# Performance work log

Measured on AMD Instinct MI355X. Metric: run time of the kernel, lower is better.

Reference implementation:

```python
import jax, jax.numpy as jnp
import numpy as np


def setup_inputs() -> dict:
    key = jax.random.key(0)
    ks = jax.random.split(key, 6)
    N, Tx, Ty = 8, 1024, 128
    enc_dim, dec_dim, Ca = 512, 1024, 128
    sc = 0.02
    return {
        "h": jax.random.normal(ks[0], (N, Tx, enc_dim), jnp.float32),
        "s": jax.random.normal(ks[1], (N, Ty, dec_dim), jnp.float32),
        "Wh": jax.random.normal(ks[2], (enc_dim, Ca), jnp.float32) * sc,
        "Ws": jax.random.normal(ks[3], (dec_dim, Ca), jnp.float32) * sc,
        "b": jax.random.normal(ks[4], (Ca,), jnp.float32) * sc,
        "v": jax.random.normal(ks[5], (Ca,), jnp.float32) * sc,
    }


def reference(h, s, Wh, Ws, b, v):
    # W([h;s]) + b == h@Wh + s@Ws + b (split of the concat Linear weight)
    ph = jnp.einsum("nxc,ca->nxa", h, Wh)            # (N, Tx, Ca)
    ps = jnp.einsum("nyd,da->nya", s, Ws) + b        # (N, Ty, Ca)
    # broadcast-add -> tanh -> dot with v : (N, Ty, Tx)
    e = jnp.einsum("nyxa,a->nyx", jnp.tanh(ps[:, :, None, :] + ph[:, None, :, :]), v)
    return jax.nn.softmax(e, axis=-1)                # attention over Tx
```

## Files before the change

kernel.cpp:

```cpp
#include <hip/hip_runtime.h>
#include <stdint.h>


typedef float  f32x4  __attribute__((ext_vector_type(4)));
typedef __bf16 bf16x8 __attribute__((ext_vector_type(8)));

#define LOG2E     1.4426950408889634f
#define TWO_LOG2E 2.8853900817779268f

__global__ void __launch_bounds__(256) transpose_cast(
    const float* __restrict__ Wh, const float* __restrict__ Ws,
    __bf16* __restrict__ WhT, __bf16* __restrict__ WsT)
{
    int bid = blockIdx.x;
    const float* src; __bf16* dst; int K, c0;
    if (bid < 8) { src = Wh; dst = WhT; K = 512;  c0 = bid * 64; }
    else         { src = Ws; dst = WsT; K = 1024; c0 = (bid - 8) * 64; }
    __shared__ float tile[64][129];
    int t = threadIdx.x;
    for (int i = 0; i < 8192; i += 256) {
        int idx = i + t;
        int r = idx >> 7, col = idx & 127;
        tile[r][col] = src[(size_t)(c0 + r) * 128 + col];
    }
    __syncthreads();
    for (int i = 0; i < 8192; i += 256) {
        int idx = i + t;
        int a = idx >> 6, cc = idx & 63;
        dst[(size_t)a * K + c0 + cc] = (__bf16)tile[cc][a];
    }
}

__global__ void __launch_bounds__(256) gemm_fused(
    const __bf16* __restrict__ WhT, const __bf16* __restrict__ WsT,
    const float* __restrict__ h, const float* __restrict__ s,
    float* __restrict__ Eph, float* __restrict__ Eps,
    const float* __restrict__ bias)
{
    int bid = blockIdx.x;
    int tid = threadIdx.x, lane = tid & 63, w = tid >> 6;
    int mbase = (w & 1) * 64;
    const __bf16* A; const float* B; float* Cp; int K; bool isPs;
    int colg;
    if (bid < 256) {
        isPs = false; A = WhT; B = h; K = 512;
        colg = bid * 32 + (w >> 1) * 16;
        int n = colg >> 10, x = colg & 1023;
        Cp = Eph + (size_t)n * 131072 + x;
    } else {
        isPs = true; A = WsT; B = s; K = 1024;
        colg = (bid - 256) * 32 + (w >> 1) * 16;
        Cp = Eps + colg;
    }
    int q = lane >> 4;
    const float*  Bp = B + (size_t)(colg + (lane & 15)) * K + q * 8;
    const __bf16* Ap = A + (size_t)(mbase + (lane & 15)) * K + q * 8;

    f32x4 acc[4] = {};
    float4 b0 = *(const float4*)(Bp);
    float4 b1 = *(const float4*)(Bp + 4);
    bf16x8 a_[4];
    #pragma unroll
    for (int i = 0; i < 4; ++i) a_[i] = *(const bf16x8*)(Ap + (size_t)i * 16 * K);

    for (int k0 = 0; k0 < K; k0 += 32) {
        int kn = k0 + 32; if (kn > K - 32) kn = K - 32;
        float4 nb0 = *(const float4*)(Bp + kn);
        float4 nb1 = *(const float4*)(Bp + kn + 4);
        bf16x8 na[4];
        #pragma unroll
        for (int i = 0; i < 4; ++i)
            na[i] = *(const bf16x8*)(Ap + (size_t)i * 16 * K + kn);
        bf16x8 bf;
        bf[0] = (__bf16)b0.x; bf[1] = (__bf16)b0.y;
        bf[2] = (__bf16)b0.z; bf[3] = (__bf16)b0.w;
        bf[4] = (__bf16)b1.x; bf[5] = (__bf16)b1.y;
        bf[6] = (__bf16)b1.z; bf[7] = (__bf16)b1.w;
        #pragma unroll
        for (int i = 0; i < 4; ++i)
            acc[i] = __builtin_amdgcn_mfma_f32_16x16x32_bf16(a_[i], bf, acc[i], 0, 0, 0);
        b0 = nb0; b1 = nb1;
        #pragma unroll
        for (int i = 0; i < 4; ++i) a_[i] = na[i];
    }

    int col = lane & 15;
    #pragma unroll
    for (int i = 0; i < 4; ++i) {
        #pragma unroll
        for (int r = 0; r < 4; ++r) {
            int m = mbase + i * 16 + q * 4 + r;
            float vv = acc[i][r];
            if (isPs) vv += bias[m];
            Cp[(size_t)m * 1024 + col] =
                __builtin_amdgcn_exp2f(vv * TWO_LOG2E);
        }
    }
}

__global__ void __launch_bounds__(512) attn_softmax(
    const float* __restrict__ Eph, const float* __restrict__ Eps,
    const float* __restrict__ v, float* __restrict__ out)
{
    int bid = blockIdx.x;
    int n = bid >> 6, yg = bid & 63;
    int ny = n * 128 + yg * 2;
    const float2* ph2 = (const float2*)(Eph + (size_t)n * 131072);
    int t = threadIdx.x;

    __shared__ float4 pv_s[128];
    __shared__ float wred[2][8];
    __shared__ float VsumS;

    if (t < 128) {
        float2 p = *(const float2*)(Eps + (size_t)t * 1024 + ny);
        float4 pk; pk.x = p.x; pk.y = p.y; pk.z = v[t]; pk.w = 0.f;
        pv_s[t] = pk;
    }
    if (t >= 448) {
        int l = t - 448;
        float vv = v[l] + v[l + 64];
        for (int m = 32; m; m >>= 1) vv += __shfl_xor(vv, m);
        if (l == 0) VsumS = vv;
    }
    __syncthreads();
    float Vsum = VsumS;

    float acc00 = 0.f, acc01 = 0.f, acc10 = 0.f, acc11 = 0.f;
    #pragma unroll 2
    for (int a = 0; a < 128; a += 4) {
        float4 q0 = pv_s[a + 0], q1 = pv_s[a + 1];
        float4 q2 = pv_s[a + 2], q3 = pv_s[a + 3];
        float2 p0 = ph2[(a + 0) * 512 + t];
        float2 p1 = ph2[(a + 1) * 512 + t];
        float2 p2 = ph2[(a + 2) * 512 + t];
        float2 p3 = ph2[(a + 3) * 512 + t];
        auto comb = [&](float e0, float e1, float e2, float e3,
                        float h0, float h1, float h2, float h3, float& acc) {
            float w0 = fmaf(e0, h0, 1.f);
            float w1 = fmaf(e1, h1, 1.f);
            float w2 = fmaf(e2, h2, 1.f);
            float w3 = fmaf(e3, h3, 1.f);
            float d01 = w0 * w1, d23 = w2 * w3;
            float n01 = fmaf(q1.z, w0, q0.z * w1);
            float n23 = fmaf(q3.z, w2, q2.z * w3);
            float dd = d01 * d23;
            float nn = fmaf(n23, d01, n01 * d23);
            acc = fmaf(nn, __builtin_amdgcn_rcpf(dd), acc);
        };
        comb(q0.x, q1.x, q2.x, q3.x, p0.x, p1.x, p2.x, p3.x, acc00);
        comb(q0.x, q1.x, q2.x, q3.x, p0.y, p1.y, p2.y, p3.y, acc01);
        comb(q0.y, q1.y, q2.y, q3.y, p0.x, p1.x, p2.x, p3.x, acc10);
        comb(q0.y, q1.y, q2.y, q3.y, p0.y, p1.y, p2.y, p3.y, acc11);
    }
    float e00 = fmaf(-2.f, acc00, Vsum);
    float e01 = fmaf(-2.f, acc01, Vsum);
    float e10 = fmaf(-2.f, acc10, Vsum);
    float e11 = fmaf(-2.f, acc11, Vsum);

    int lane = t & 63, wv = t >> 6;
    float mx0 = fmaxf(e00, e01), mx1 = fmaxf(e10, e11);
    for (int m = 32; m; m >>= 1) {
        mx0 = fmaxf(mx0, __shfl_xor(mx0, m));
        mx1 = fmaxf(mx1, __shfl_xor(mx1, m));
    }
    if (lane == 0) { wred[0][wv] = mx0; wred[1][wv] = mx1; }
    __syncthreads();
    mx0 = wred[0][0]; mx1 = wred[1][0];
    #pragma unroll
    for (int i = 1; i < 8; ++i) {
        mx0 = fmaxf(mx0, wred[0][i]);
        mx1 = fmaxf(mx1, wred[1][i]);
    }
    __syncthreads();
    float s00 = __builtin_amdgcn_exp2f((e00 - mx0) * LOG2E);
    float s01 = __builtin_amdgcn_exp2f((e01 - mx0) * LOG2E);
    float s10 = __builtin_amdgcn_exp2f((e10 - mx1) * LOG2E);
    float s11 = __builtin_amdgcn_exp2f((e11 - mx1) * LOG2E);
    float sm0 = s00 + s01, sm1 = s10 + s11;
    for (int m = 32; m; m >>= 1) {
        sm0 += __shfl_xor(sm0, m);
        sm1 += __shfl_xor(sm1, m);
    }
    if (lane == 0) { wred[0][wv] = sm0; wred[1][wv] = sm1; }
    __syncthreads();
    sm0 = 0.f; sm1 = 0.f;
    #pragma unroll
    for (int i = 0; i < 8; ++i) { sm0 += wred[0][i]; sm1 += wred[1][i]; }
    float r0 = __builtin_amdgcn_rcpf(sm0);
    float r1 = __builtin_amdgcn_rcpf(sm1);
    float2 o0; o0.x = s00 * r0; o0.y = s01 * r0;
    float2 o1; o1.x = s10 * r1; o1.y = s11 * r1;
    ((float2*)(out + (size_t)(ny + 0) * 1024))[t] = o0;
    ((float2*)(out + (size_t)(ny + 1) * 1024))[t] = o1;
}

extern "C" void kernel_launch(void* const* d_in, const int* in_sizes, int n_in,
                              void* d_out, int out_size, void* d_ws, size_t ws_size,
                              hipStream_t stream) {
    const float* h  = (const float*)d_in[0];
    const float* s  = (const float*)d_in[1];
    const float* Wh = (const float*)d_in[2];
    const float* Ws = (const float*)d_in[3];
    const float* b  = (const float*)d_in[4];
    const float* v  = (const float*)d_in[5];
    float* out = (float*)d_out;

    char* ws = (char*)d_ws;
    float*  Eph = (float*)ws;
    float*  Eps = (float*)(ws + (4u << 20));
    __bf16* WhT = (__bf16*)(ws + (4u << 20) + (512u << 10));
    __bf16* WsT = WhT + (size_t)128 * 512;

    transpose_cast<<<24, 256, 0, stream>>>(Wh, Ws, WhT, WsT);
    gemm_fused<<<288, 256, 0, stream>>>(WhT, WsT, h, s, Eph, Eps, b);
    attn_softmax<<<512, 512, 0, stream>>>(Eph, Eps, v, out);
}
```

Measured before the change: 132.1 us.

## Split-K the s-projection GEMM and move its bias/exp into the softmax kernel

```diff
diff --git a/kernel.cpp b/kernel.cpp
--- a/kernel.cpp
+++ b/kernel.cpp
@@ -34,73 +34,78 @@
 __global__ void __launch_bounds__(256) gemm_fused(
     const __bf16* __restrict__ WhT, const __bf16* __restrict__ WsT,
     const float* __restrict__ h, const float* __restrict__ s,
-    float* __restrict__ Eph, float* __restrict__ Eps,
-    const float* __restrict__ bias)
+    float* __restrict__ Eph, float* __restrict__ psPart)
 {
     int bid = blockIdx.x;
     int tid = threadIdx.x, lane = tid & 63, w = tid >> 6;
-    int mbase = (w & 1) * 64;
-    const __bf16* A; const float* B; float* Cp; int K; bool isPs;
-    int colg;
-    if (bid < 256) {
-        isPs = false; A = WhT; B = h; K = 512;
-        colg = bid * 32 + (w >> 1) * 16;
+    int mq = w * 32;
+    int q = lane >> 4, c = lane & 15;
+
+    const __bf16* A; const float* B; float* Cp; int K, kbase, colg; bool isPs;
+    if (bid < 512) {
+        isPs = false; A = WhT; B = h; K = 512; kbase = 0;
+        colg = bid * 16;
         int n = colg >> 10, x = colg & 1023;
         Cp = Eph + (size_t)n * 131072 + x;
     } else {
         isPs = true; A = WsT; B = s; K = 1024;
-        colg = (bid - 256) * 32 + (w >> 1) * 16;
-        Cp = Eps + colg;
-    }
-    int q = lane >> 4;
-    const float*  Bp = B + (size_t)(colg + (lane & 15)) * K + q * 8;
-    const __bf16* Ap = A + (size_t)(mbase + (lane & 15)) * K + q * 8;
-
-    f32x4 acc[4] = {};
-    float4 b0 = *(const float4*)(Bp);
-    float4 b1 = *(const float4*)(Bp + 4);
-    bf16x8 a_[4];
-    #pragma unroll
-    for (int i = 0; i < 4; ++i) a_[i] = *(const bf16x8*)(Ap + (size_t)i * 16 * K);
-
-    for (int k0 = 0; k0 < K; k0 += 32) {
-        int kn = k0 + 32; if (kn > K - 32) kn = K - 32;
-        float4 nb0 = *(const float4*)(Bp + kn);
-        float4 nb1 = *(const float4*)(Bp + kn + 4);
-        bf16x8 na[4];
-        #pragma unroll
-        for (int i = 0; i < 4; ++i)
-            na[i] = *(const bf16x8*)(Ap + (size_t)i * 16 * K + kn);
+        int b2 = bid - 512;
+        int half = b2 & 1; kbase = half * 512;
+        colg = (b2 >> 1) * 16;
+        Cp = psPart + (size_t)half * 131072 + colg;
+    }
+
+    const float*  Bp = B + (size_t)(colg + c) * K + kbase + q * 8;
+    const __bf16* Ap = A + (size_t)(mq + c) * K + kbase + q * 8;
+
+    f32x4 acc0 = {}, acc1 = {};
+    float4 b0s[4], b1s[4];
+    bf16x8 a0s[4], a1s[4];
+    #pragma unroll
+    for (int p = 0; p < 4; ++p) {
+        int k = p * 32;
+        b0s[p] = *(const float4*)(Bp + k);
+        b1s[p] = *(const float4*)(Bp + k + 4);
+        a0s[p] = *(const bf16x8*)(Ap + k);
+        a1s[p] = *(const bf16x8*)(Ap + (size_t)16 * K + k);
+    }
+    #pragma unroll
+    for (int it = 0; it < 16; ++it) {
+        int cur = it & 3;
+        float4 b0 = b0s[cur], b1 = b1s[cur];
         bf16x8 bf;
         bf[0] = (__bf16)b0.x; bf[1] = (__bf16)b0.y;
         bf[2] = (__bf16)b0.z; bf[3] = (__bf16)b0.w;
         bf[4] = (__bf16)b1.x; bf[5] = (__bf16)b1.y;
         bf[6] = (__bf16)b1.z; bf[7] = (__bf16)b1.w;
-        #pragma unroll
-        for (int i = 0; i < 4; ++i)
-            acc[i] = __builtin_amdgcn_mfma_f32_16x16x32_bf16(a_[i], bf, acc[i], 0, 0, 0);
-        b0 = nb0; b1 = nb1;
-        #pragma unroll
-        for (int i = 0; i < 4; ++i) a_[i] = na[i];
-    }
-
-    int col = lane & 15;
-    #pragma unroll
-    for (int i = 0; i < 4; ++i) {
+        acc0 = __builtin_amdgcn_mfma_f32_16x16x32_bf16(a0s[cur], bf, acc0, 0, 0, 0);
+        acc1 = __builtin_amdgcn_mfma_f32_16x16x32_bf16(a1s[cur], bf, acc1, 0, 0, 0);
+        if (it + 4 < 16) {
+            int k = (it + 4) * 32;
+            b0s[cur] = *(const float4*)(Bp + k);
+            b1s[cur] = *(const float4*)(Bp + k + 4);
+            a0s[cur] = *(const bf16x8*)(Ap + k);
+            a1s[cur] = *(const bf16x8*)(Ap + (size_t)16 * K + k);
+        }
+    }
+
+    #pragma unroll
+    for (int i = 0; i < 2; ++i) {
+        f32x4 av = i ? acc1 : acc0;
         #pragma unroll
         for (int r = 0; r < 4; ++r) {
-            int m = mbase + i * 16 + q * 4 + r;
-            float vv = acc[i][r];
-            if (isPs) vv += bias[m];
-            Cp[(size_t)m * 1024 + col] =
-                __builtin_amdgcn_exp2f(vv * TWO_LOG2E);
+            int m = mq + i * 16 + q * 4 + r;
+            if (isPs) Cp[(size_t)m * 1024 + c] = av[r];
+            else      Cp[(size_t)m * 1024 + c] =
+                          __builtin_amdgcn_exp2f(av[r] * TWO_LOG2E);
         }
     }
 }
 
 __global__ void __launch_bounds__(512) attn_softmax(
-    const float* __restrict__ Eph, const float* __restrict__ Eps,
-    const float* __restrict__ v, float* __restrict__ out)
+    const float* __restrict__ Eph, const float* __restrict__ psPart,
+    const float* __restrict__ bias, const float* __restrict__ v,
+    float* __restrict__ out)
 {
     int bid = blockIdx.x;
     int n = bid >> 6, yg = bid & 63;
@@ -113,8 +118,13 @@
     __shared__ float VsumS;
 
     if (t < 128) {
-        float2 p = *(const float2*)(Eps + (size_t)t * 1024 + ny);
-        float4 pk; pk.x = p.x; pk.y = p.y; pk.z = v[t]; pk.w = 0.f;
+        float2 pa = *(const float2*)(psPart + (size_t)t * 1024 + ny);
+        float2 pb = *(const float2*)(psPart + 131072 + (size_t)t * 1024 + ny);
+        float bb = bias[t];
+        float4 pk;
+        pk.x = __builtin_amdgcn_exp2f((pa.x + pb.x + bb) * TWO_LOG2E);
+        pk.y = __builtin_amdgcn_exp2f((pa.y + pb.y + bb) * TWO_LOG2E);
+        pk.z = v[t]; pk.w = 0.f;
         pv_s[t] = pk;
     }
     if (t >= 448) {
@@ -207,12 +217,12 @@
     float* out = (float*)d_out;
 
     char* ws = (char*)d_ws;
-    float*  Eph = (float*)ws;
-    float*  Eps = (float*)(ws + (4u << 20));
-    __bf16* WhT = (__bf16*)(ws + (4u << 20) + (512u << 10));
-    __bf16* WsT = WhT + (size_t)128 * 512;
+    float*  Eph    = (float*)ws;
+    float*  psPart = (float*)(ws + (4u << 20));
+    __bf16* WhT    = (__bf16*)(ws + (5u << 20));
+    __bf16* WsT    = WhT + (size_t)128 * 512;
 
     transpose_cast<<<24, 256, 0, stream>>>(Wh, Ws, WhT, WsT);
-    gemm_fused<<<288, 256, 0, stream>>>(WhT, WsT, h, s, Eph, Eps, b);
-    attn_softmax<<<512, 512, 0, stream>>>(Eph, Eps, v, out);
-}
+    gemm_fused<<<640, 256, 0, stream>>>(WhT, WsT, h, s, Eph, psPart);
+    attn_softmax<<<512, 512, 0, stream>>>(Eph, psPart, b, v, out);
+}
```

Result: faster. 118.9 us (-10.0%).
